# Kernel tuning notes

Measured on AMD Instinct MI355X. Metric: run time of the kernel, lower is better.

## Reference

```python
import jax, jax.numpy as jnp
import numpy as np

B, DIN, DOUT, NW = 32768, 768, 768, 48
NH = NW // 3  # num_haar == num_mexican == num_morlet == 16 for NW=48
OMEGA0 = 5.0
LN_EPS = 1e-5


def setup_inputs() -> dict:
    key = jax.random.key(0)
    ks = jax.random.split(key, 6)
    x = jax.random.normal(ks[0], (B, DIN), dtype=jnp.float32)
    # kaiming-normal-ish fan_in init for linear layers, zero bias
    W = jax.random.normal(ks[1], (DOUT, DIN), dtype=jnp.float32) / np.sqrt(DIN)
    b = jnp.zeros((DOUT,), jnp.float32)
    Wp = jax.random.normal(ks[2], (NW, DIN), dtype=jnp.float32) / np.sqrt(DIN)
    bp = jnp.zeros((NW,), jnp.float32)
    Wc = jax.random.normal(ks[3], (DOUT, NW), dtype=jnp.float32) / np.sqrt(NW)
    bc = jnp.zeros((DOUT,), jnp.float32)
    # mixed-type init: per-family logspace scales / linspace translations
    scales = jnp.asarray(np.concatenate([
        np.logspace(-0.5, 0.5, NH),
        np.logspace(-0.3, 0.7, NH),
        np.logspace(-0.3, 0.7, NW - 2 * NH)]), jnp.float32)
    translations = jnp.asarray(np.concatenate([
        np.linspace(-1.5, 1.5, NH),
        np.linspace(-1.5, 1.5, NH),
        np.linspace(-1.5, 1.5, NW - 2 * NH)]), jnp.float32)
    gamma = jnp.ones((DOUT,), jnp.float32)
    beta = jnp.zeros((DOUT,), jnp.float32)
    return {"x": x, "W": W, "b": b, "Wp": Wp, "bp": bp, "Wc": Wc,
            "bc": bc, "scales": scales, "translations": translations,
            "gamma": gamma, "beta": beta}


def _wavelet_basis(s):
    # s: [B, NW] already scaled/translated; columns split by family
    dt = s.dtype
    sh = s[:, :NH]
    haar = (((sh >= 0) & (sh < 0.5)).astype(dt)
            - ((sh >= 0.5) & (sh < 1.0)).astype(dt))
    sm = s[:, NH:2 * NH]
    mexican = (1.0 - sm * sm) * jnp.exp(-0.5 * sm * sm)
    so = s[:, 2 * NH:]
    morlet = jnp.cos(OMEGA0 * so) * jnp.exp(-0.5 * so * so)
    return jnp.concatenate([haar, mexican, morlet], axis=1)


def reference(x, W, b, Wp, bp, Wc, bc, scales, translations, gamma, beta):
    direct = x @ W.T + b                              # [B, DOUT]
    wi = x @ Wp.T + bp                                # [B, NW]
    s = (wi - translations) / scales                  # [B, NW]
    wav = jax.nn.gelu(_wavelet_basis(s), approximate=False)
    wpath = wav @ Wc.T + bc                           # [B, DOUT]
    h = direct + wpath
    mu = jnp.mean(h, axis=-1, keepdims=True)
    var = jnp.mean((h - mu) ** 2, axis=-1, keepdims=True)
    return (h - mu) * jax.lax.rsqrt(var + LN_EPS) * gamma + beta
```

## Files before the change

kernel.cpp:

```cpp
#include <hip/hip_runtime.h>
#include <math.h>


#define B_SZ  32768
#define DIN   768
#define DOUT  768
#define NWAV  48

#define WF_OFF   0
#define WPH_OFF  589824
#define WPL_OFF  638976
#define WCF_OFF  688128

typedef short bf16x8 __attribute__((ext_vector_type(8)));
typedef float f32x16 __attribute__((ext_vector_type(16)));

__device__ __forceinline__ float bf2f(short u) {
    union { unsigned int i; float f; } v;
    v.i = ((unsigned int)(unsigned short)u) << 16;
    return v.f;
}
__device__ __forceinline__ short f2bf(float f) {
    union { float f; unsigned int i; } v; v.f = f;
    unsigned int r = v.i + 0x7FFFu + ((v.i >> 16) & 1u);
    return (short)(r >> 16);
}

__global__ __launch_bounds__(256) void pack_kernel(
    const float* __restrict__ W, const float* __restrict__ Wp,
    const float* __restrict__ Wc, short* __restrict__ ws)
{
    const int gw = (blockIdx.x * 256 + threadIdx.x) >> 6;
    const int L  = threadIdx.x & 63;
    const int lm = L & 31, half = L >> 5;

    if (gw < 1152) {
        const int cb = gw / 48, kb = gw % 48;
        const int row = cb * 32 + lm;
        const int k = kb * 16 + half * 8;
        bf16x8 o;
#pragma unroll
        for (int j = 0; j < 8; j++) o[j] = f2bf(W[(size_t)row * DIN + k + j]);
        *reinterpret_cast<bf16x8*>(&ws[WF_OFF + (size_t)gw * 512 + L * 8]) = o;
    } else if (gw < 1248) {
        const int t = gw - 1152;
        const int ct = t / 48, kb = t % 48;
        const int j = ct * 32 + lm;
        const int k = kb * 16 + half * 8;
        bf16x8 h, l;
#pragma unroll
        for (int jj = 0; jj < 8; jj++) {
            float v = (j < NWAV) ? Wp[(size_t)j * DIN + k + jj] : 0.f;
            const short hh = f2bf(v);
            h[jj] = hh;
            l[jj] = f2bf(v - bf2f(hh));
        }
        *reinterpret_cast<bf16x8*>(&ws[WPH_OFF + (size_t)t * 512 + L * 8]) = h;
        *reinterpret_cast<bf16x8*>(&ws[WPL_OFF + (size_t)t * 512 + L * 8]) = l;
    } else if (gw < 1320) {
        const int t = gw - 1248;
        const int cb = t / 3, kb = t % 3;
        const int row = cb * 32 + lm;
        const int k = kb * 16 + half * 8;
        bf16x8 o;
#pragma unroll
        for (int jj = 0; jj < 8; jj++) o[jj] = f2bf(Wc[(size_t)row * NWAV + k + jj]);
        *reinterpret_cast<bf16x8*>(&ws[WCF_OFF + (size_t)t * 512 + L * 8]) = o;
    }
}

__global__ __launch_bounds__(512, 2) void fused_kernel(
    const float* __restrict__ x, const short* __restrict__ ws,
    const float* __restrict__ Wp,
    const float* __restrict__ bp, const float* __restrict__ sc,
    const float* __restrict__ tr,
    const float* __restrict__ bb, const float* __restrict__ bc,
    const float* __restrict__ gm, const float* __restrict__ bt,
    float* __restrict__ out)
{
    __shared__ __align__(16) short xh[2][64 * 72];
    __shared__ __align__(16) short xl[2][64 * 72];
    __shared__ float redS[64 * 8], redQ[64 * 8];
    __shared__ float muA[64], rsA[64];

    const short* WF  = ws + WF_OFF;
    const short* WPH = ws + WPH_OFF;
    const short* WPL = ws + WPL_OFF;
    const short* WCF = ws + WCF_OFF;

    const int tid = threadIdx.x;
    const int r0  = blockIdx.x * 64;
    const int wv  = tid >> 6, L = tid & 63;
    const int lm  = L & 31, half = L >> 5;

    f32x16 acc[2][3];
#pragma unroll
    for (int rt = 0; rt < 2; rt++)
#pragma unroll
        for (int ct = 0; ct < 3; ct++)
#pragma unroll
            for (int g = 0; g < 16; g++) acc[rt][ct][g] = 0.f;
    f32x16 wacc;
#pragma unroll
    for (int g = 0; g < 16; g++) wacc[g] = 0.f;

    const int wrt = wv & 1, wct = wv >> 1;

    const int srow = tid >> 3;
    const int sk   = (tid & 7) * 8;

    {
        const float4* xp = reinterpret_cast<const float4*>(&x[(size_t)(r0 + srow) * DIN + sk]);
        const float4 v0 = xp[0], v1 = xp[1];
        const float f[8] = {v0.x, v0.y, v0.z, v0.w, v1.x, v1.y, v1.z, v1.w};
        bf16x8 hh, ll;
#pragma unroll
        for (int i = 0; i < 8; i++) {
            const short h = f2bf(f[i]);
            hh[i] = h;
            ll[i] = f2bf(f[i] - bf2f(h));
        }
        *reinterpret_cast<bf16x8*>(&xh[0][srow * 72 + sk]) = hh;
        *reinterpret_cast<bf16x8*>(&xl[0][srow * 72 + sk]) = ll;
    }
    __syncthreads();

    for (int k0i = 0; k0i < 12; ++k0i) {
        const int cur = k0i & 1;
        float4 v0, v1;
        if (k0i < 11) {
            const float4* xp = reinterpret_cast<const float4*>(
                &x[(size_t)(r0 + srow) * DIN + (k0i + 1) * 64 + sk]);
            v0 = xp[0]; v1 = xp[1];
        }
        const int kb0 = k0i * 4;

#pragma unroll
        for (int ks = 0; ks < 4; ++ks) {
            const bf16x8 a0 = *reinterpret_cast<bf16x8*>(&xh[cur][lm * 72 + ks * 16 + half * 8]);
            const bf16x8 a1 = *reinterpret_cast<bf16x8*>(&xh[cur][(32 + lm) * 72 + ks * 16 + half * 8]);
#pragma unroll
            for (int ct = 0; ct < 3; ++ct) {
                const bf16x8 b = *reinterpret_cast<const bf16x8*>(
                    &WF[((size_t)((wv * 3 + ct) * 48 + kb0 + ks)) * 512 + L * 8]);
                acc[0][ct] = __builtin_amdgcn_mfma_f32_32x32x16_bf16(a0, b, acc[0][ct], 0, 0, 0);
                acc[1][ct] = __builtin_amdgcn_mfma_f32_32x32x16_bf16(a1, b, acc[1][ct], 0, 0, 0);
            }
        }

        if (wv < 4) {
#pragma unroll
            for (int ks = 0; ks < 4; ++ks) {
                const bf16x8 ah = *reinterpret_cast<bf16x8*>(&xh[cur][(wrt * 32 + lm) * 72 + ks * 16 + half * 8]);
                const bf16x8 al = *reinterpret_cast<bf16x8*>(&xl[cur][(wrt * 32 + lm) * 72 + ks * 16 + half * 8]);
                const bf16x8 bh = *reinterpret_cast<const bf16x8*>(
                    &WPH[((size_t)(wct * 48 + kb0 + ks)) * 512 + L * 8]);
                const bf16x8 bl = *reinterpret_cast<const bf16x8*>(
                    &WPL[((size_t)(wct * 48 + kb0 + ks)) * 512 + L * 8]);
                wacc = __builtin_amdgcn_mfma_f32_32x32x16_bf16(ah, bl, wacc, 0, 0, 0);
                wacc = __builtin_amdgcn_mfma_f32_32x32x16_bf16(al, bh, wacc, 0, 0, 0);
                wacc = __builtin_amdgcn_mfma_f32_32x32x16_bf16(ah, bh, wacc, 0, 0, 0);
            }
        }

        if (k0i < 11) {
            const float f[8] = {v0.x, v0.y, v0.z, v0.w, v1.x, v1.y, v1.z, v1.w};
            bf16x8 hh, ll;
#pragma unroll
            for (int i = 0; i < 8; i++) {
                const short h = f2bf(f[i]);
                hh[i] = h;
                ll[i] = f2bf(f[i] - bf2f(h));
            }
            *reinterpret_cast<bf16x8*>(&xh[1 - cur][srow * 72 + sk]) = hh;
            *reinterpret_cast<bf16x8*>(&xl[1 - cur][srow * 72 + sk]) = ll;
        }
        __syncthreads();
    }

    short* wavL = &xh[0][0];
    if (wv < 4) {
        const int j = wct * 32 + lm;
        if (j < NWAV) {
            const float bpv = bp[j], scv = sc[j], trv = tr[j];
#pragma unroll
            for (int g = 0; g < 16; ++g) {
                const int rowl = wrt * 32 + (g & 3) + 8 * (g >> 2) + 4 * half;
                const float wi = wacc[g] + bpv;
                const float s = (wi - trv) / scv;
                float w;
                if (j < 16) {
                    const float dmin = fminf(fabsf(s), fminf(fabsf(s - 0.5f), fabsf(s - 1.0f)));
                    if (dmin < 2e-4f) {
                        const float* xr = &x[(size_t)(r0 + rowl) * DIN];
                        const float* wr = &Wp[(size_t)j * DIN];
                        double a0 = 0.0, a1 = 0.0, a2 = 0.0, a3 = 0.0;
                        for (int k = 0; k < DIN; k += 4) {
                            a0 = fma((double)xr[k + 0], (double)wr[k + 0], a0);
                            a1 = fma((double)xr[k + 1], (double)wr[k + 1], a1);
                            a2 = fma((double)xr[k + 2], (double)wr[k + 2], a2);
                            a3 = fma((double)xr[k + 3], (double)wr[k + 3], a3);
                        }
                        const double wid = ((a0 + a1) + (a2 + a3)) + (double)bpv;
                        const double sd = (wid - (double)trv) / (double)scv;
                        w = (sd >= 0.0 && sd < 0.5) ? 1.f : ((sd >= 0.5 && sd < 1.0) ? -1.f : 0.f);
                    } else {
                        w = (s >= 0.f && s < 0.5f) ? 1.f : ((s >= 0.5f && s < 1.f) ? -1.f : 0.f);
                    }
                } else if (j < 32) {
                    w = (1.f - s * s) * expf(-0.5f * s * s);
                } else {
                    w = cosf(5.f * s) * expf(-0.5f * s * s);
                }
                const float gel = 0.5f * w * (1.f + erff(w * 0.70710678118654752f));
                wavL[rowl * 72 + j] = f2bf(gel);
            }
        }
    }
    __syncthreads();

#pragma unroll
    for (int ks = 0; ks < 3; ++ks) {
        const bf16x8 a0 = *reinterpret_cast<bf16x8*>(&wavL[lm * 72 + ks * 16 + half * 8]);
        const bf16x8 a1 = *reinterpret_cast<bf16x8*>(&wavL[(32 + lm) * 72 + ks * 16 + half * 8]);
#pragma unroll
        for (int ct = 0; ct < 3; ++ct) {
            const bf16x8 b = *reinterpret_cast<const bf16x8*>(
                &WCF[((size_t)((wv * 3 + ct) * 3 + ks)) * 512 + L * 8]);
            acc[0][ct] = __builtin_amdgcn_mfma_f32_32x32x16_bf16(a0, b, acc[0][ct], 0, 0, 0);
            acc[1][ct] = __builtin_amdgcn_mfma_f32_32x32x16_bf16(a1, b, acc[1][ct], 0, 0, 0);
        }
    }

    float bias[3], gmv[3], btv[3];
#pragma unroll
    for (int ct = 0; ct < 3; ++ct) {
        const int col = wv * 96 + ct * 32 + lm;
        bias[ct] = bb[col] + bc[col];
        gmv[ct] = gm[col];
        btv[ct] = bt[col];
    }
#pragma unroll
    for (int rt = 0; rt < 2; ++rt) {
#pragma unroll
        for (int g = 0; g < 16; ++g) {
            const float v0 = acc[rt][0][g] + bias[0];
            const float v1 = acc[rt][1][g] + bias[1];
            const float v2 = acc[rt][2][g] + bias[2];
            acc[rt][0][g] = v0; acc[rt][1][g] = v1; acc[rt][2][g] = v2;
            float s1 = v0 + v1 + v2;
            float s2 = v0 * v0 + v1 * v1 + v2 * v2;
            s1 += __shfl_xor(s1, 1);  s2 += __shfl_xor(s2, 1);
            s1 += __shfl_xor(s1, 2);  s2 += __shfl_xor(s2, 2);
            s1 += __shfl_xor(s1, 4);  s2 += __shfl_xor(s2, 4);
            s1 += __shfl_xor(s1, 8);  s2 += __shfl_xor(s2, 8);
            s1 += __shfl_xor(s1, 16); s2 += __shfl_xor(s2, 16);
            if (lm == 0) {
                const int rowl = rt * 32 + (g & 3) + 8 * (g >> 2) + 4 * half;
                redS[rowl * 8 + wv] = s1;
                redQ[rowl * 8 + wv] = s2;
            }
        }
    }
    __syncthreads();
    if (tid < 64) {
        float S = 0.f, Q = 0.f;
#pragma unroll
        for (int i = 0; i < 8; i++) { S += redS[tid * 8 + i]; Q += redQ[tid * 8 + i]; }
        const float mu = S * (1.f / 768.f);
        const float var = Q * (1.f / 768.f) - mu * mu;
        muA[tid] = mu;
        rsA[tid] = rsqrtf(var + 1e-5f);
    }
    __syncthreads();

#pragma unroll
    for (int rt = 0; rt < 2; ++rt) {
#pragma unroll
        for (int g = 0; g < 16; ++g) {
            const int rowl = rt * 32 + (g & 3) + 8 * (g >> 2) + 4 * half;
            const float mu = muA[rowl], rs = rsA[rowl];
            float* orow = &out[(size_t)(r0 + rowl) * DOUT + wv * 96 + lm];
#pragma unroll
            for (int ct = 0; ct < 3; ++ct) {
                orow[ct * 32] = (acc[rt][ct][g] - mu) * rs * gmv[ct] + btv[ct];
            }
        }
    }
}

extern "C" void kernel_launch(void* const* d_in, const int* in_sizes, int n_in,
                              void* d_out, int out_size, void* d_ws, size_t ws_size,
                              hipStream_t stream)
{
    const float* x  = (const float*)d_in[0];
    const float* W  = (const float*)d_in[1];
    const float* b  = (const float*)d_in[2];
    const float* Wp = (const float*)d_in[3];
    const float* bp = (const float*)d_in[4];
    const float* Wc = (const float*)d_in[5];
    const float* bc = (const float*)d_in[6];
    const float* sc = (const float*)d_in[7];
    const float* tr = (const float*)d_in[8];
    const float* gm = (const float*)d_in[9];
    const float* bt = (const float*)d_in[10];
    float* out = (float*)d_out;
    short* ws  = (short*)d_ws;

    pack_kernel<<<dim3(330), dim3(256), 0, stream>>>(W, Wp, Wc, ws);
    fused_kernel<<<dim3(B_SZ / 64), dim3(512), 0, stream>>>(
        x, ws, Wp, bp, sc, tr, b, bc, gm, bt, out);
}
```

Baseline: 307.1 us.

## Split fused kernel into wavelet, column-tiled GEMM, and LayerNorm kernels

Replaces the single fused kernel with three kernels. The first computes the wavelet-projection GEMM and the GELU basis and writes bf16 results to workspace. The second is a GEMM tiled 128 rows by 128 columns, spread over 6 column blocks, that writes pre-norm activations to the output. The third applies LayerNorm in place. The goal is better MFMA tiling and occupancy for the large GEMM. The cost is that x is read about 7 times and the full output goes through an extra write-read-write round trip in HBM.

```diff
diff --git a/kernel.cpp b/kernel.cpp
--- a/kernel.cpp
+++ b/kernel.cpp
@@ -11,6 +11,7 @@
 #define WPH_OFF  589824
 #define WPL_OFF  638976
 #define WCF_OFF  688128
+#define WAV_OFF  724992
 
 typedef short bf16x8 __attribute__((ext_vector_type(8)));
 typedef float f32x16 __attribute__((ext_vector_type(16)));
@@ -69,223 +70,259 @@
     }
 }
 
-__global__ __launch_bounds__(512, 2) void fused_kernel(
-    const float* __restrict__ x, const short* __restrict__ ws,
-    const float* __restrict__ Wp,
+__global__ __launch_bounds__(256) void wav_kernel(
+    const float* __restrict__ x, const float* __restrict__ Wp,
     const float* __restrict__ bp, const float* __restrict__ sc,
-    const float* __restrict__ tr,
-    const float* __restrict__ bb, const float* __restrict__ bc,
-    const float* __restrict__ gm, const float* __restrict__ bt,
-    float* __restrict__ out)
-{
-    __shared__ __align__(16) short xh[2][64 * 72];
-    __shared__ __align__(16) short xl[2][64 * 72];
-    __shared__ float redS[64 * 8], redQ[64 * 8];
-    __shared__ float muA[64], rsA[64];
-
-    const short* WF  = ws + WF_OFF;
+    const float* __restrict__ tr, short* __restrict__ ws)
+{
+    __shared__ __align__(16) short xh[64 * 72];
+    __shared__ __align__(16) short xl[64 * 72];
+
     const short* WPH = ws + WPH_OFF;
     const short* WPL = ws + WPL_OFF;
-    const short* WCF = ws + WCF_OFF;
+    short* wav = ws + WAV_OFF;
 
     const int tid = threadIdx.x;
     const int r0  = blockIdx.x * 64;
     const int wv  = tid >> 6, L = tid & 63;
     const int lm  = L & 31, half = L >> 5;
-
-    f32x16 acc[2][3];
+    const int rt  = wv & 1, ct = wv >> 1;
+
+    f32x16 wacc;
+#pragma unroll
+    for (int g = 0; g < 16; g++) wacc[g] = 0.f;
+
+    const int srow = tid >> 2;
+    const int sk   = (tid & 3) * 16;
+
+    for (int k0i = 0; k0i < 12; ++k0i) {
+        const float4* xp = reinterpret_cast<const float4*>(
+            &x[(size_t)(r0 + srow) * DIN + k0i * 64 + sk]);
+        const float4 v0 = xp[0], v1 = xp[1], v2 = xp[2], v3 = xp[3];
+        __syncthreads();
+        {
+            const float f[16] = {v0.x, v0.y, v0.z, v0.w, v1.x, v1.y, v1.z, v1.w,
+                                 v2.x, v2.y, v2.z, v2.w, v3.x, v3.y, v3.z, v3.w};
+            bf16x8 hh0, ll0, hh1, ll1;
+#pragma unroll
+            for (int i = 0; i < 8; i++) {
+                short h = f2bf(f[i]);
+                hh0[i] = h; ll0[i] = f2bf(f[i] - bf2f(h));
+                h = f2bf(f[8 + i]);
+                hh1[i] = h; ll1[i] = f2bf(f[8 + i] - bf2f(h));
+            }
+            *reinterpret_cast<bf16x8*>(&xh[srow * 72 + sk])     = hh0;
+            *reinterpret_cast<bf16x8*>(&xh[srow * 72 + sk + 8]) = hh1;
+            *reinterpret_cast<bf16x8*>(&xl[srow * 72 + sk])     = ll0;
+            *reinterpret_cast<bf16x8*>(&xl[srow * 72 + sk + 8]) = ll1;
+        }
+        __syncthreads();
+        const int kb0 = k0i * 4;
+#pragma unroll
+        for (int ks = 0; ks < 4; ++ks) {
+            const bf16x8 ah = *reinterpret_cast<bf16x8*>(&xh[(rt * 32 + lm) * 72 + ks * 16 + half * 8]);
+            const bf16x8 al = *reinterpret_cast<bf16x8*>(&xl[(rt * 32 + lm) * 72 + ks * 16 + half * 8]);
+            const bf16x8 bh = *reinterpret_cast<const bf16x8*>(&WPH[((size_t)(ct * 48 + kb0 + ks)) * 512 + L * 8]);
+            const bf16x8 bl = *reinterpret_cast<const bf16x8*>(&WPL[((size_t)(ct * 48 + kb0 + ks)) * 512 + L * 8]);
+            wacc = __builtin_amdgcn_mfma_f32_32x32x16_bf16(ah, bl, wacc, 0, 0, 0);
+            wacc = __builtin_amdgcn_mfma_f32_32x32x16_bf16(al, bh, wacc, 0, 0, 0);
+            wacc = __builtin_amdgcn_mfma_f32_32x32x16_bf16(ah, bh, wacc, 0, 0, 0);
+        }
+    }
+
+    const int j = ct * 32 + lm;
+    if (j < NWAV) {
+        const float bpv = bp[j], scv = sc[j], trv = tr[j];
+#pragma unroll
+        for (int g = 0; g < 16; ++g) {
+            const int rowl = rt * 32 + (g & 3) + 8 * (g >> 2) + 4 * half;
+            const float wi = wacc[g] + bpv;
+            const float s = (wi - trv) / scv;
+            float w;
+            if (j < 16) {
+                const float dmin = fminf(fabsf(s), fminf(fabsf(s - 0.5f), fabsf(s - 1.0f)));
+                if (dmin < 2e-4f) {
+                    const float* xr = &x[(size_t)(r0 + rowl) * DIN];
+                    const float* wr = &Wp[(size_t)j * DIN];
+                    double a0 = 0.0, a1 = 0.0, a2 = 0.0, a3 = 0.0;
+                    for (int k = 0; k < DIN; k += 4) {
+                        a0 = fma((double)xr[k + 0], (double)wr[k + 0], a0);
+                        a1 = fma((double)xr[k + 1], (double)wr[k + 1], a1);
+                        a2 = fma((double)xr[k + 2], (double)wr[k + 2], a2);
+                        a3 = fma((double)xr[k + 3], (double)wr[k + 3], a3);
+                    }
+                    const double wid = ((a0 + a1) + (a2 + a3)) + (double)bpv;
+                    const double sd = (wid - (double)trv) / (double)scv;
+                    w = (sd >= 0.0 && sd < 0.5) ? 1.f : ((sd >= 0.5 && sd < 1.0) ? -1.f : 0.f);
+                } else {
+                    w = (s >= 0.f && s < 0.5f) ? 1.f : ((s >= 0.5f && s < 1.f) ? -1.f : 0.f);
+                }
+            } else if (j < 32) {
+                w = (1.f - s * s) * expf(-0.5f * s * s);
+            } else {
+                w = cosf(5.f * s) * expf(-0.5f * s * s);
+            }
+            const float gel = 0.5f * w * (1.f + erff(w * 0.70710678118654752f));
+            wav[(size_t)(r0 + rowl) * NWAV + j] = f2bf(gel);
+        }
+    }
+}
+
+__global__ __launch_bounds__(256, 3) void gemm_kernel(
+    const float* __restrict__ x, const short* __restrict__ ws,
+    const float* __restrict__ bb, const float* __restrict__ bc,
+    float* __restrict__ hout)
+{
+    __shared__ __align__(16) short xs[2][128 * 72];
+
+    const short* WF  = ws + WF_OFF;
+    const short* WCF = ws + WCF_OFF;
+    const short* wavg = ws + WAV_OFF;
+
+    const int tid  = threadIdx.x;
+    const int bx   = blockIdx.x;
+    const int colb = bx % 6;
+    const int r0   = (bx / 6) * 128;
+    const int wv   = tid >> 6, L = tid & 63;
+    const int lm   = L & 31, half = L >> 5;
+    const int wm   = wv >> 1, wn = wv & 1;
+
+    f32x16 acc[2][2];
 #pragma unroll
     for (int rt = 0; rt < 2; rt++)
 #pragma unroll
-        for (int ct = 0; ct < 3; ct++)
+        for (int ct = 0; ct < 2; ct++)
 #pragma unroll
             for (int g = 0; g < 16; g++) acc[rt][ct][g] = 0.f;
-    f32x16 wacc;
-#pragma unroll
-    for (int g = 0; g < 16; g++) wacc[g] = 0.f;
-
-    const int wrt = wv & 1, wct = wv >> 1;
-
-    const int srow = tid >> 3;
-    const int sk   = (tid & 7) * 8;
+
+    const int srow = tid >> 1;
+    const int sk   = (tid & 1) * 32;
 
     {
         const float4* xp = reinterpret_cast<const float4*>(&x[(size_t)(r0 + srow) * DIN + sk]);
-        const float4 v0 = xp[0], v1 = xp[1];
-        const float f[8] = {v0.x, v0.y, v0.z, v0.w, v1.x, v1.y, v1.z, v1.w};
-        bf16x8 hh, ll;
-#pragma unroll
-        for (int i = 0; i < 8; i++) {
-            const short h = f2bf(f[i]);
-            hh[i] = h;
-            ll[i] = f2bf(f[i] - bf2f(h));
-        }
-        *reinterpret_cast<bf16x8*>(&xh[0][srow * 72 + sk]) = hh;
-        *reinterpret_cast<bf16x8*>(&xl[0][srow * 72 + sk]) = ll;
+#pragma unroll
+        for (int u = 0; u < 4; ++u) {
+            const float4 a = xp[2 * u], b2 = xp[2 * u + 1];
+            bf16x8 hh;
+            hh[0] = f2bf(a.x); hh[1] = f2bf(a.y); hh[2] = f2bf(a.z); hh[3] = f2bf(a.w);
+            hh[4] = f2bf(b2.x); hh[5] = f2bf(b2.y); hh[6] = f2bf(b2.z); hh[7] = f2bf(b2.w);
+            *reinterpret_cast<bf16x8*>(&xs[0][srow * 72 + sk + u * 8]) = hh;
+        }
     }
     __syncthreads();
 
     for (int k0i = 0; k0i < 12; ++k0i) {
         const int cur = k0i & 1;
-        float4 v0, v1;
+        float4 pf[8];
         if (k0i < 11) {
             const float4* xp = reinterpret_cast<const float4*>(
                 &x[(size_t)(r0 + srow) * DIN + (k0i + 1) * 64 + sk]);
-            v0 = xp[0]; v1 = xp[1];
+#pragma unroll
+            for (int u = 0; u < 8; ++u) pf[u] = xp[u];
         }
         const int kb0 = k0i * 4;
-
 #pragma unroll
         for (int ks = 0; ks < 4; ++ks) {
-            const bf16x8 a0 = *reinterpret_cast<bf16x8*>(&xh[cur][lm * 72 + ks * 16 + half * 8]);
-            const bf16x8 a1 = *reinterpret_cast<bf16x8*>(&xh[cur][(32 + lm) * 72 + ks * 16 + half * 8]);
-#pragma unroll
-            for (int ct = 0; ct < 3; ++ct) {
+            const bf16x8 a0 = *reinterpret_cast<bf16x8*>(&xs[cur][(wm * 64 + lm) * 72 + ks * 16 + half * 8]);
+            const bf16x8 a1 = *reinterpret_cast<bf16x8*>(&xs[cur][(wm * 64 + 32 + lm) * 72 + ks * 16 + half * 8]);
+#pragma unroll
+            for (int ct = 0; ct < 2; ++ct) {
+                const int cb = colb * 4 + wn * 2 + ct;
                 const bf16x8 b = *reinterpret_cast<const bf16x8*>(
-                    &WF[((size_t)((wv * 3 + ct) * 48 + kb0 + ks)) * 512 + L * 8]);
+                    &WF[((size_t)(cb * 48 + kb0 + ks)) * 512 + L * 8]);
                 acc[0][ct] = __builtin_amdgcn_mfma_f32_32x32x16_bf16(a0, b, acc[0][ct], 0, 0, 0);
                 acc[1][ct] = __builtin_amdgcn_mfma_f32_32x32x16_bf16(a1, b, acc[1][ct], 0, 0, 0);
             }
         }
-
-        if (wv < 4) {
-#pragma unroll
-            for (int ks = 0; ks < 4; ++ks) {
-                const bf16x8 ah = *reinterpret_cast<bf16x8*>(&xh[cur][(wrt * 32 + lm) * 72 + ks * 16 + half * 8]);
-                const bf16x8 al = *reinterpret_cast<bf16x8*>(&xl[cur][(wrt * 32 + lm) * 72 + ks * 16 + half * 8]);
-                const bf16x8 bh = *reinterpret_cast<const bf16x8*>(
-                    &WPH[((size_t)(wct * 48 + kb0 + ks)) * 512 + L * 8]);
-                const bf16x8 bl = *reinterpret_cast<const bf16x8*>(
-                    &WPL[((size_t)(wct * 48 + kb0 + ks)) * 512 + L * 8]);
-                wacc = __builtin_amdgcn_mfma_f32_32x32x16_bf16(ah, bl, wacc, 0, 0, 0);
-                wacc = __builtin_amdgcn_mfma_f32_32x32x16_bf16(al, bh, wacc, 0, 0, 0);
-                wacc = __builtin_amdgcn_mfma_f32_32x32x16_bf16(ah, bh, wacc, 0, 0, 0);
-            }
-        }
-
         if (k0i < 11) {
-            const float f[8] = {v0.x, v0.y, v0.z, v0.w, v1.x, v1.y, v1.z, v1.w};
-            bf16x8 hh, ll;
-#pragma unroll
-            for (int i = 0; i < 8; i++) {
-                const short h = f2bf(f[i]);
-                hh[i] = h;
-                ll[i] = f2bf(f[i] - bf2f(h));
-            }
-            *reinterpret_cast<bf16x8*>(&xh[1 - cur][srow * 72 + sk]) = hh;
-            *reinterpret_cast<bf16x8*>(&xl[1 - cur][srow * 72 + sk]) = ll;
+#pragma unroll
+            for (int u = 0; u < 4; ++u) {
+                const float4 a = pf[2 * u], b2 = pf[2 * u + 1];
+                bf16x8 hh;
+                hh[0] = f2bf(a.x); hh[1] = f2bf(a.y); hh[2] = f2bf(a.z); hh[3] = f2bf(a.w);
+                hh[4] = f2bf(b2.x); hh[5] = f2bf(b2.y); hh[6] = f2bf(b2.z); hh[7] = f2bf(b2.w);
+                *reinterpret_cast<bf16x8*>(&xs[1 - cur][srow * 72 + sk + u * 8]) = hh;
+            }
         }
         __syncthreads();
     }
 
-    short* wavL = &xh[0][0];
-    if (wv < 4) {
-        const int j = wct * 32 + lm;
-        if (j < NWAV) {
-            const float bpv = bp[j], scv = sc[j], trv = tr[j];
-#pragma unroll
-            for (int g = 0; g < 16; ++g) {
-                const int rowl = wrt * 32 + (g & 3) + 8 * (g >> 2) + 4 * half;
-                const float wi = wacc[g] + bpv;
-                const float s = (wi - trv) / scv;
-                float w;
-                if (j < 16) {
-                    const float dmin = fminf(fabsf(s), fminf(fabsf(s - 0.5f), fabsf(s - 1.0f)));
-                    if (dmin < 2e-4f) {
-                        const float* xr = &x[(size_t)(r0 + rowl) * DIN];
-                        const float* wr = &Wp[(size_t)j * DIN];
-                        double a0 = 0.0, a1 = 0.0, a2 = 0.0, a3 = 0.0;
-                        for (int k = 0; k < DIN; k += 4) {
-                            a0 = fma((double)xr[k + 0], (double)wr[k + 0], a0);
-                            a1 = fma((double)xr[k + 1], (double)wr[k + 1], a1);
-                            a2 = fma((double)xr[k + 2], (double)wr[k + 2], a2);
-                            a3 = fma((double)xr[k + 3], (double)wr[k + 3], a3);
-                        }
-                        const double wid = ((a0 + a1) + (a2 + a3)) + (double)bpv;
-                        const double sd = (wid - (double)trv) / (double)scv;
-                        w = (sd >= 0.0 && sd < 0.5) ? 1.f : ((sd >= 0.5 && sd < 1.0) ? -1.f : 0.f);
-                    } else {
-                        w = (s >= 0.f && s < 0.5f) ? 1.f : ((s >= 0.5f && s < 1.f) ? -1.f : 0.f);
-                    }
-                } else if (j < 32) {
-                    w = (1.f - s * s) * expf(-0.5f * s * s);
-                } else {
-                    w = cosf(5.f * s) * expf(-0.5f * s * s);
-                }
-                const float gel = 0.5f * w * (1.f + erff(w * 0.70710678118654752f));
-                wavL[rowl * 72 + j] = f2bf(gel);
-            }
-        }
+    {
+        const int row = tid >> 1, part = tid & 1;
+        const int4* src = reinterpret_cast<const int4*>(&wavg[(size_t)(r0 + row) * NWAV + part * 24]);
+        const int4 a = src[0], b2 = src[1], c = src[2];
+        int4* dst = reinterpret_cast<int4*>(&xs[0][row * 72 + part * 24]);
+        dst[0] = a; dst[1] = b2; dst[2] = c;
+        const int4 zz = {0, 0, 0, 0};
+        *reinterpret_cast<int4*>(&xs[0][row * 72 + 48 + part * 8]) = zz;
     }
     __syncthreads();
-
 #pragma unroll
     for (int ks = 0; ks < 3; ++ks) {
-        const bf16x8 a0 = *reinterpret_cast<bf16x8*>(&wavL[lm * 72 + ks * 16 + half * 8]);
-        const bf16x8 a1 = *reinterpret_cast<bf16x8*>(&wavL[(32 + lm) * 72 + ks * 16 + half * 8]);
-#pragma unroll
-        for (int ct = 0; ct < 3; ++ct) {
+        const bf16x8 a0 = *reinterpret_cast<bf16x8*>(&xs[0][(wm * 64 + lm) * 72 + ks * 16 + half * 8]);
+        const bf16x8 a1 = *reinterpret_cast<bf16x8*>(&xs[0][(wm * 64 + 32 + lm) * 72 + ks * 16 + half * 8]);
+#pragma unroll
+        for (int ct = 0; ct < 2; ++ct) {
+            const int cb = colb * 4 + wn * 2 + ct;
             const bf16x8 b = *reinterpret_cast<const bf16x8*>(
-                &WCF[((size_t)((wv * 3 + ct) * 3 + ks)) * 512 + L * 8]);
+                &WCF[((size_t)(cb * 3 + ks)) * 512 + L * 8]);
             acc[0][ct] = __builtin_amdgcn_mfma_f32_32x32x16_bf16(a0, b, acc[0][ct], 0, 0, 0);
             acc[1][ct] = __builtin_amdgcn_mfma_f32_32x32x16_bf16(a1, b, acc[1][ct], 0, 0, 0);
         }
     }
 
-    float bias[3], gmv[3], btv[3];
-#pragma unroll
-    for (int ct = 0; ct < 3; ++ct) {
-        const int col = wv * 96 + ct * 32 + lm;
-        bias[ct] = bb[col] + bc[col];
-        gmv[ct] = gm[col];
-        btv[ct] = bt[col];
-    }
-#pragma unroll
-    for (int rt = 0; rt < 2; ++rt) {
-#pragma unroll
-        for (int g = 0; g < 16; ++g) {
-            const float v0 = acc[rt][0][g] + bias[0];
-            const float v1 = acc[rt][1][g] + bias[1];
-            const float v2 = acc[rt][2][g] + bias[2];
-            acc[rt][0][g] = v0; acc[rt][1][g] = v1; acc[rt][2][g] = v2;
-            float s1 = v0 + v1 + v2;
-            float s2 = v0 * v0 + v1 * v1 + v2 * v2;
-            s1 += __shfl_xor(s1, 1);  s2 += __shfl_xor(s2, 1);
-            s1 += __shfl_xor(s1, 2);  s2 += __shfl_xor(s2, 2);
-            s1 += __shfl_xor(s1, 4);  s2 += __shfl_xor(s2, 4);
-            s1 += __shfl_xor(s1, 8);  s2 += __shfl_xor(s2, 8);
-            s1 += __shfl_xor(s1, 16); s2 += __shfl_xor(s2, 16);
-            if (lm == 0) {
-                const int rowl = rt * 32 + (g & 3) + 8 * (g >> 2) + 4 * half;
-                redS[rowl * 8 + wv] = s1;
-                redQ[rowl * 8 + wv] = s2;
-            }
-        }
-    }
-    __syncthreads();
-    if (tid < 64) {
-        float S = 0.f, Q = 0.f;
-#pragma unroll
-        for (int i = 0; i < 8; i++) { S += redS[tid * 8 + i]; Q += redQ[tid * 8 + i]; }
-        const float mu = S * (1.f / 768.f);
-        const float var = Q * (1.f / 768.f) - mu * mu;
-        muA[tid] = mu;
-        rsA[tid] = rsqrtf(var + 1e-5f);
-    }
-    __syncthreads();
-
-#pragma unroll
-    for (int rt = 0; rt < 2; ++rt) {
-#pragma unroll
-        for (int g = 0; g < 16; ++g) {
-            const int rowl = rt * 32 + (g & 3) + 8 * (g >> 2) + 4 * half;
-            const float mu = muA[rowl], rs = rsA[rowl];
-            float* orow = &out[(size_t)(r0 + rowl) * DOUT + wv * 96 + lm];
-#pragma unroll
-            for (int ct = 0; ct < 3; ++ct) {
-                orow[ct * 32] = (acc[rt][ct][g] - mu) * rs * gmv[ct] + btv[ct];
-            }
-        }
+#pragma unroll
+    for (int ct = 0; ct < 2; ++ct) {
+        const int colg = (colb * 4 + wn * 2 + ct) * 32 + lm;
+        const float bias = bb[colg] + bc[colg];
+#pragma unroll
+        for (int rt = 0; rt < 2; ++rt) {
+#pragma unroll
+            for (int g = 0; g < 16; ++g) {
+                const int row = r0 + wm * 64 + rt * 32 + (g & 3) + 8 * (g >> 2) + 4 * half;
+                hout[(size_t)row * DOUT + colg] = acc[rt][ct][g] + bias;
+            }
+        }
+    }
+}
+
+__global__ __launch_bounds__(256) void ln_kernel(
+    float* __restrict__ io, const float* __restrict__ gm,
+    const float* __restrict__ bt)
+{
+    const int row = blockIdx.x * 4 + (threadIdx.x >> 6);
+    const int l   = threadIdx.x & 63;
+    float* rp = &io[(size_t)row * DOUT];
+
+    float4 v[3];
+#pragma unroll
+    for (int c = 0; c < 3; ++c)
+        v[c] = *reinterpret_cast<const float4*>(&rp[l * 4 + c * 256]);
+
+    float s1 = 0.f, s2 = 0.f;
+#pragma unroll
+    for (int c = 0; c < 3; ++c) {
+        s1 += v[c].x + v[c].y + v[c].z + v[c].w;
+        s2 += v[c].x * v[c].x + v[c].y * v[c].y + v[c].z * v[c].z + v[c].w * v[c].w;
+    }
+#pragma unroll
+    for (int d = 1; d < 64; d <<= 1) {
+        s1 += __shfl_xor(s1, d);
+        s2 += __shfl_xor(s2, d);
+    }
+    const float mu = s1 * (1.f / 768.f);
+    const float rs = rsqrtf(s2 * (1.f / 768.f) - mu * mu + 1e-5f);
+
+#pragma unroll
+    for (int c = 0; c < 3; ++c) {
+        const float4 g = *reinterpret_cast<const float4*>(&gm[l * 4 + c * 256]);
+        const float4 b = *reinterpret_cast<const float4*>(&bt[l * 4 + c * 256]);
+        float4 o;
+        o.x = (v[c].x - mu) * rs * g.x + b.x;
+        o.y = (v[c].y - mu) * rs * g.y + b.y;
+        o.z = (v[c].z - mu) * rs * g.z + b.z;
+        o.w = (v[c].w - mu) * rs * g.w + b.w;
+        *reinterpret_cast<float4*>(&rp[l * 4 + c * 256]) = o;
     }
 }
 
@@ -308,6 +345,7 @@
     short* ws  = (short*)d_ws;
 
     pack_kernel<<<dim3(330), dim3(256), 0, stream>>>(W, Wp, Wc, ws);
-    fused_kernel<<<dim3(B_SZ / 64), dim3(512), 0, stream>>>(
-        x, ws, Wp, bp, sc, tr, b, bc, gm, bt, out);
-}
+    wav_kernel<<<dim3(B_SZ / 64), dim3(256), 0, stream>>>(x, Wp, bp, sc, tr, ws);
+    gemm_kernel<<<dim3((B_SZ / 128) * 6), dim3(256), 0, stream>>>(x, ws, b, bc, out);
+    ln_kernel<<<dim3(B_SZ / 4), dim3(256), 0, stream>>>(out, gm, bt);
+}
```

After: 389.3 us. +26.8%, slower.

## Use 1024-thread blocks with split-K wavelet projection and per-row-group waves

Applied to the files above, without the earlier changes.

Doubles the block to 16 waves, so each wave computes one 32-row by 96-column tile of the direct GEMM instead of two row tiles. This halves accumulator registers per wave. The 48-wide wavelet projection is now split across all 16 waves by K quarter, and partial sums are reduced through shared memory before the wavelet/GELU stage. That stage is now spread over all waves, with each lane handling one wavelet column for four rows. The aim is more waves per CU and better balance in the wavelet work. The costs are extra barriers, an LDS reduction, and a larger shared buffer that may limit occupancy.

```diff
diff --git a/kernel.cpp b/kernel.cpp
--- a/kernel.cpp
+++ b/kernel.cpp
@@ -69,7 +69,7 @@
     }
 }
 
-__global__ __launch_bounds__(512, 2) void fused_kernel(
+__global__ __launch_bounds__(1024) void fused_kernel(
     const float* __restrict__ x, const short* __restrict__ ws,
     const float* __restrict__ Wp,
     const float* __restrict__ bp, const float* __restrict__ sc,
@@ -78,10 +78,14 @@
     const float* __restrict__ gm, const float* __restrict__ bt,
     float* __restrict__ out)
 {
-    __shared__ __align__(16) short xh[2][64 * 72];
-    __shared__ __align__(16) short xl[2][64 * 72];
+    __shared__ __align__(16) short xbuf[73728];
+    __shared__ __align__(16) short wavL[64 * 72];
     __shared__ float redS[64 * 8], redQ[64 * 8];
     __shared__ float muA[64], rsA[64];
+
+    short (*xh)[64 * 72] = reinterpret_cast<short (*)[64 * 72]>(&xbuf[0]);
+    short (*xl)[64 * 72] = reinterpret_cast<short (*)[64 * 72]>(&xbuf[2 * 64 * 72]);
+    float* wiS = reinterpret_cast<float*>(&xbuf[0]);
 
     const short* WF  = ws + WF_OFF;
     const short* WPH = ws + WPH_OFF;
@@ -92,174 +96,172 @@
     const int r0  = blockIdx.x * 64;
     const int wv  = tid >> 6, L = tid & 63;
     const int lm  = L & 31, half = L >> 5;
-
-    f32x16 acc[2][3];
-#pragma unroll
-    for (int rt = 0; rt < 2; rt++)
-#pragma unroll
-        for (int ct = 0; ct < 3; ct++)
-#pragma unroll
-            for (int g = 0; g < 16; g++) acc[rt][ct][g] = 0.f;
+    const int rg  = wv >> 3, cg = wv & 7;
+    const int kq  = wv >> 2;
+    const int wrg = (wv & 3) >> 1, wch = wv & 1;
+
+    f32x16 acc[3];
+#pragma unroll
+    for (int ct = 0; ct < 3; ct++)
+#pragma unroll
+        for (int g = 0; g < 16; g++) acc[ct][g] = 0.f;
     f32x16 wacc;
 #pragma unroll
     for (int g = 0; g < 16; g++) wacc[g] = 0.f;
 
-    const int wrt = wv & 1, wct = wv >> 1;
-
-    const int srow = tid >> 3;
-    const int sk   = (tid & 7) * 8;
+    const int srow = tid >> 4;
+    const int skc  = (tid & 15) * 4;
 
     {
-        const float4* xp = reinterpret_cast<const float4*>(&x[(size_t)(r0 + srow) * DIN + sk]);
-        const float4 v0 = xp[0], v1 = xp[1];
-        const float f[8] = {v0.x, v0.y, v0.z, v0.w, v1.x, v1.y, v1.z, v1.w};
-        bf16x8 hh, ll;
-#pragma unroll
-        for (int i = 0; i < 8; i++) {
-            const short h = f2bf(f[i]);
-            hh[i] = h;
-            ll[i] = f2bf(f[i] - bf2f(h));
-        }
-        *reinterpret_cast<bf16x8*>(&xh[0][srow * 72 + sk]) = hh;
-        *reinterpret_cast<bf16x8*>(&xl[0][srow * 72 + sk]) = ll;
+        const float4 v = *reinterpret_cast<const float4*>(&x[(size_t)(r0 + srow) * DIN + skc]);
+        const float f[4] = {v.x, v.y, v.z, v.w};
+        short hh[4], ll[4];
+#pragma unroll
+        for (int i = 0; i < 4; i++) {
+            hh[i] = f2bf(f[i]);
+            ll[i] = f2bf(f[i] - bf2f(hh[i]));
+        }
+        *reinterpret_cast<short4*>(&xh[0][srow * 72 + skc]) = *reinterpret_cast<short4*>(hh);
+        *reinterpret_cast<short4*>(&xl[0][srow * 72 + skc]) = *reinterpret_cast<short4*>(ll);
     }
     __syncthreads();
 
     for (int k0i = 0; k0i < 12; ++k0i) {
         const int cur = k0i & 1;
-        float4 v0, v1;
-        if (k0i < 11) {
-            const float4* xp = reinterpret_cast<const float4*>(
-                &x[(size_t)(r0 + srow) * DIN + (k0i + 1) * 64 + sk]);
-            v0 = xp[0]; v1 = xp[1];
-        }
+        float4 pf;
+        if (k0i < 11)
+            pf = *reinterpret_cast<const float4*>(&x[(size_t)(r0 + srow) * DIN + (k0i + 1) * 64 + skc]);
+
         const int kb0 = k0i * 4;
-
 #pragma unroll
         for (int ks = 0; ks < 4; ++ks) {
-            const bf16x8 a0 = *reinterpret_cast<bf16x8*>(&xh[cur][lm * 72 + ks * 16 + half * 8]);
-            const bf16x8 a1 = *reinterpret_cast<bf16x8*>(&xh[cur][(32 + lm) * 72 + ks * 16 + half * 8]);
+            const bf16x8 a0 = *reinterpret_cast<bf16x8*>(&xh[cur][(rg * 32 + lm) * 72 + ks * 16 + half * 8]);
 #pragma unroll
             for (int ct = 0; ct < 3; ++ct) {
                 const bf16x8 b = *reinterpret_cast<const bf16x8*>(
-                    &WF[((size_t)((wv * 3 + ct) * 48 + kb0 + ks)) * 512 + L * 8]);
-                acc[0][ct] = __builtin_amdgcn_mfma_f32_32x32x16_bf16(a0, b, acc[0][ct], 0, 0, 0);
-                acc[1][ct] = __builtin_amdgcn_mfma_f32_32x32x16_bf16(a1, b, acc[1][ct], 0, 0, 0);
+                    &WF[((size_t)((cg * 3 + ct) * 48 + kb0 + ks)) * 512 + L * 8]);
+                acc[ct] = __builtin_amdgcn_mfma_f32_32x32x16_bf16(a0, b, acc[ct], 0, 0, 0);
             }
         }
-
-        if (wv < 4) {
+        if (k0i >= kq * 3 && k0i < kq * 3 + 3) {
 #pragma unroll
             for (int ks = 0; ks < 4; ++ks) {
-                const bf16x8 ah = *reinterpret_cast<bf16x8*>(&xh[cur][(wrt * 32 + lm) * 72 + ks * 16 + half * 8]);
-                const bf16x8 al = *reinterpret_cast<bf16x8*>(&xl[cur][(wrt * 32 + lm) * 72 + ks * 16 + half * 8]);
+                const bf16x8 ah = *reinterpret_cast<bf16x8*>(&xh[cur][(wrg * 32 + lm) * 72 + ks * 16 + half * 8]);
+                const bf16x8 al = *reinterpret_cast<bf16x8*>(&xl[cur][(wrg * 32 + lm) * 72 + ks * 16 + half * 8]);
                 const bf16x8 bh = *reinterpret_cast<const bf16x8*>(
-                    &WPH[((size_t)(wct * 48 + kb0 + ks)) * 512 + L * 8]);
+                    &WPH[((size_t)(wch * 48 + kb0 + ks)) * 512 + L * 8]);
                 const bf16x8 bl = *reinterpret_cast<const bf16x8*>(
-                    &WPL[((size_t)(wct * 48 + kb0 + ks)) * 512 + L * 8]);
+                    &WPL[((size_t)(wch * 48 + kb0 + ks)) * 512 + L * 8]);
                 wacc = __builtin_amdgcn_mfma_f32_32x32x16_bf16(ah, bl, wacc, 0, 0, 0);
                 wacc = __builtin_amdgcn_mfma_f32_32x32x16_bf16(al, bh, wacc, 0, 0, 0);
                 wacc = __builtin_amdgcn_mfma_f32_32x32x16_bf16(ah, bh, wacc, 0, 0, 0);
             }
         }
-
         if (k0i < 11) {
-            const float f[8] = {v0.x, v0.y, v0.z, v0.w, v1.x, v1.y, v1.z, v1.w};
-            bf16x8 hh, ll;
-#pragma unroll
-            for (int i = 0; i < 8; i++) {
-                const short h = f2bf(f[i]);
-                hh[i] = h;
-                ll[i] = f2bf(f[i] - bf2f(h));
+            const float f[4] = {pf.x, pf.y, pf.z, pf.w};
+            short hh[4], ll[4];
+#pragma unroll
+            for (int i = 0; i < 4; i++) {
+                hh[i] = f2bf(f[i]);
+                ll[i] = f2bf(f[i] - bf2f(hh[i]));
             }
-            *reinterpret_cast<bf16x8*>(&xh[1 - cur][srow * 72 + sk]) = hh;
-            *reinterpret_cast<bf16x8*>(&xl[1 - cur][srow * 72 + sk]) = ll;
+            *reinterpret_cast<short4*>(&xh[1 - cur][srow * 72 + skc]) = *reinterpret_cast<short4*>(hh);
+            *reinterpret_cast<short4*>(&xl[1 - cur][srow * 72 + skc]) = *reinterpret_cast<short4*>(ll);
         }
         __syncthreads();
     }
 
-    short* wavL = &xh[0][0];
-    if (wv < 4) {
-        const int j = wct * 32 + lm;
-        if (j < NWAV) {
-            const float bpv = bp[j], scv = sc[j], trv = tr[j];
-#pragma unroll
-            for (int g = 0; g < 16; ++g) {
-                const int rowl = wrt * 32 + (g & 3) + 8 * (g >> 2) + 4 * half;
-                const float wi = wacc[g] + bpv;
-                const float s = (wi - trv) / scv;
-                float w;
-                if (j < 16) {
-                    const float dmin = fminf(fabsf(s), fminf(fabsf(s - 0.5f), fabsf(s - 1.0f)));
-                    if (dmin < 2e-4f) {
-                        const float* xr = &x[(size_t)(r0 + rowl) * DIN];
-                        const float* wr = &Wp[(size_t)j * DIN];
-                        double a0 = 0.0, a1 = 0.0, a2 = 0.0, a3 = 0.0;
-                        for (int k = 0; k < DIN; k += 4) {
-                            a0 = fma((double)xr[k + 0], (double)wr[k + 0], a0);
-                            a1 = fma((double)xr[k + 1], (double)wr[k + 1], a1);
-                            a2 = fma((double)xr[k + 2], (double)wr[k + 2], a2);
-                            a3 = fma((double)xr[k + 3], (double)wr[k + 3], a3);
-                        }
-                        const double wid = ((a0 + a1) + (a2 + a3)) + (double)bpv;
-                        const double sd = (wid - (double)trv) / (double)scv;
-                        w = (sd >= 0.0 && sd < 0.5) ? 1.f : ((sd >= 0.5 && sd < 1.0) ? -1.f : 0.f);
-                    } else {
-                        w = (s >= 0.f && s < 0.5f) ? 1.f : ((s >= 0.5f && s < 1.f) ? -1.f : 0.f);
+    if (kq < 2) {
+#pragma unroll
+        for (int g = 0; g < 16; ++g) {
+            const int row = wrg * 32 + (g & 3) + 8 * (g >> 2) + 4 * half;
+            wiS[(size_t)kq * 4096 + row * 64 + wch * 32 + lm] = wacc[g];
+        }
+    }
+    __syncthreads();
+    if (kq >= 2) {
+#pragma unroll
+        for (int g = 0; g < 16; ++g) {
+            const int row = wrg * 32 + (g & 3) + 8 * (g >> 2) + 4 * half;
+            wiS[(size_t)(kq - 2) * 4096 + row * 64 + wch * 32 + lm] += wacc[g];
+        }
+    }
+    __syncthreads();
+
+    const int j = L;
+    if (j < NWAV) {
+        const float bpv = bp[j], scv = sc[j], trv = tr[j];
+#pragma unroll
+        for (int rr = 0; rr < 4; ++rr) {
+            const int row = wv * 4 + rr;
+            const float wi = wiS[row * 64 + j] + wiS[4096 + row * 64 + j] + bpv;
+            const float s = (wi - trv) / scv;
+            float w;
+            if (j < 16) {
+                const float dmin = fminf(fabsf(s), fminf(fabsf(s - 0.5f), fabsf(s - 1.0f)));
+                if (dmin < 2e-4f) {
+                    const float* xr = &x[(size_t)(r0 + row) * DIN];
+                    const float* wr = &Wp[(size_t)j * DIN];
+                    double a0 = 0.0, a1 = 0.0, a2 = 0.0, a3 = 0.0;
+                    for (int k = 0; k < DIN; k += 4) {
+                        a0 = fma((double)xr[k + 0], (double)wr[k + 0], a0);
+                        a1 = fma((double)xr[k + 1], (double)wr[k + 1], a1);
+                        a2 = fma((double)xr[k + 2], (double)wr[k + 2], a2);
+                        a3 = fma((double)xr[k + 3], (double)wr[k + 3], a3);
                     }
-                } else if (j < 32) {
-                    w = (1.f - s * s) * expf(-0.5f * s * s);
+                    const double wid = ((a0 + a1) + (a2 + a3)) + (double)bpv;
+                    const double sd = (wid - (double)trv) / (double)scv;
+                    w = (sd >= 0.0 && sd < 0.5) ? 1.f : ((sd >= 0.5 && sd < 1.0) ? -1.f : 0.f);
                 } else {
-                    w = cosf(5.f * s) * expf(-0.5f * s * s);
+                    w = (s >= 0.f && s < 0.5f) ? 1.f : ((s >= 0.5f && s < 1.f) ? -1.f : 0.f);
                 }
-                const float gel = 0.5f * w * (1.f + erff(w * 0.70710678118654752f));
-                wavL[rowl * 72 + j] = f2bf(gel);
+            } else if (j < 32) {
+                w = (1.f - s * s) * expf(-0.5f * s * s);
+            } else {
+                w = cosf(5.f * s) * expf(-0.5f * s * s);
             }
+            const float gel = 0.5f * w * (1.f + erff(w * 0.70710678118654752f));
+            wavL[row * 72 + j] = f2bf(gel);
         }
     }
     __syncthreads();
 
 #pragma unroll
     for (int ks = 0; ks < 3; ++ks) {
-        const bf16x8 a0 = *reinterpret_cast<bf16x8*>(&wavL[lm * 72 + ks * 16 + half * 8]);
-        const bf16x8 a1 = *reinterpret_cast<bf16x8*>(&wavL[(32 + lm) * 72 + ks * 16 + half * 8]);
+        const bf16x8 a0 = *reinterpret_cast<bf16x8*>(&wavL[(rg * 32 + lm) * 72 + ks * 16 + half * 8]);
 #pragma unroll
         for (int ct = 0; ct < 3; ++ct) {
             const bf16x8 b = *reinterpret_cast<const bf16x8*>(
-                &WCF[((size_t)((wv * 3 + ct) * 3 + ks)) * 512 + L * 8]);
-            acc[0][ct] = __builtin_amdgcn_mfma_f32_32x32x16_bf16(a0, b, acc[0][ct], 0, 0, 0);
-            acc[1][ct] = __builtin_amdgcn_mfma_f32_32x32x16_bf16(a1, b, acc[1][ct], 0, 0, 0);
-        }
-    }
-
-    float bias[3], gmv[3], btv[3];
+                &WCF[((size_t)((cg * 3 + ct) * 3 + ks)) * 512 + L * 8]);
+            acc[ct] = __builtin_amdgcn_mfma_f32_32x32x16_bf16(a0, b, acc[ct], 0, 0, 0);
+        }
+    }
+
+    float bias[3], g_[3], b_[3];
 #pragma unroll
     for (int ct = 0; ct < 3; ++ct) {
-        const int col = wv * 96 + ct * 32 + lm;
+        const int col = cg * 96 + ct * 32 + lm;
         bias[ct] = bb[col] + bc[col];
-        gmv[ct] = gm[col];
-        btv[ct] = bt[col];
-    }
-#pragma unroll
-    for (int rt = 0; rt < 2; ++rt) {
-#pragma unroll
-        for (int g = 0; g < 16; ++g) {
-            const float v0 = acc[rt][0][g] + bias[0];
-            const float v1 = acc[rt][1][g] + bias[1];
-            const float v2 = acc[rt][2][g] + bias[2];
-            acc[rt][0][g] = v0; acc[rt][1][g] = v1; acc[rt][2][g] = v2;
-            float s1 = v0 + v1 + v2;
-            float s2 = v0 * v0 + v1 * v1 + v2 * v2;
-            s1 += __shfl_xor(s1, 1);  s2 += __shfl_xor(s2, 1);
-            s1 += __shfl_xor(s1, 2);  s2 += __shfl_xor(s2, 2);
-            s1 += __shfl_xor(s1, 4);  s2 += __shfl_xor(s2, 4);
-            s1 += __shfl_xor(s1, 8);  s2 += __shfl_xor(s2, 8);
-            s1 += __shfl_xor(s1, 16); s2 += __shfl_xor(s2, 16);
-            if (lm == 0) {
-                const int rowl = rt * 32 + (g & 3) + 8 * (g >> 2) + 4 * half;
-                redS[rowl * 8 + wv] = s1;
-                redQ[rowl * 8 + wv] = s2;
-            }
+        g_[ct] = gm[col];
+        b_[ct] = bt[col];
+    }
+#pragma unroll
+    for (int g = 0; g < 16; ++g) {
+        const float v0 = acc[0][g] + bias[0];
+        const float v1 = acc[1][g] + bias[1];
+        const float v2 = acc[2][g] + bias[2];
+        acc[0][g] = v0; acc[1][g] = v1; acc[2][g] = v2;
+        float s1 = v0 + v1 + v2;
+        float s2 = v0 * v0 + v1 * v1 + v2 * v2;
+        s1 += __shfl_xor(s1, 1);  s2 += __shfl_xor(s2, 1);
+        s1 += __shfl_xor(s1, 2);  s2 += __shfl_xor(s2, 2);
+        s1 += __shfl_xor(s1, 4);  s2 += __shfl_xor(s2, 4);
+        s1 += __shfl_xor(s1, 8);  s2 += __shfl_xor(s2, 8);
+        s1 += __shfl_xor(s1, 16); s2 += __shfl_xor(s2, 16);
+        if (lm == 0) {
+            const int row = rg * 32 + (g & 3) + 8 * (g >> 2) + 4 * half;
+            redS[row * 8 + cg] = s1;
+            redQ[row * 8 + cg] = s2;
         }
     }
     __syncthreads();
@@ -275,16 +277,13 @@
     __syncthreads();
 
 #pragma unroll
-    for (int rt = 0; rt < 2; ++rt) {
-#pragma unroll
-        for (int g = 0; g < 16; ++g) {
-            const int rowl = rt * 32 + (g & 3) + 8 * (g >> 2) + 4 * half;
-            const float mu = muA[rowl], rs = rsA[rowl];
-            float* orow = &out[(size_t)(r0 + rowl) * DOUT + wv * 96 + lm];
-#pragma unroll
-            for (int ct = 0; ct < 3; ++ct) {
-                orow[ct * 32] = (acc[rt][ct][g] - mu) * rs * gmv[ct] + btv[ct];
-            }
+    for (int g = 0; g < 16; ++g) {
+        const int row = rg * 32 + (g & 3) + 8 * (g >> 2) + 4 * half;
+        const float mu = muA[row], rs = rsA[row];
+        float* orow = &out[(size_t)(r0 + row) * DOUT + cg * 96 + lm];
+#pragma unroll
+        for (int ct = 0; ct < 3; ++ct) {
+            orow[ct * 32] = (acc[ct][g] - mu) * rs * g_[ct] + b_[ct];
         }
     }
 }
@@ -308,6 +307,6 @@
     short* ws  = (short*)d_ws;
 
     pack_kernel<<<dim3(330), dim3(256), 0, stream>>>(W, Wp, Wc, ws);
-    fused_kernel<<<dim3(B_SZ / 64), dim3(512), 0, stream>>>(
+    fused_kernel<<<dim3(B_SZ / 64), dim3(1024), 0, stream>>>(
         x, ws, Wp, bp, sc, tr, b, bc, gm, bt, out);
 }
```

After: 309.3 us. Within noise of the previous version (+0.7%).
